# Kernel tuning notes

Measured on AMD Instinct MI355X. Metric: run time of the kernel, lower is better.

## Reference

```python
import jax, jax.numpy as jnp
import numpy as np

KERNEL_SIZE = 5
PAD = (KERNEL_SIZE - 1) // 2  # 2
PATCH = KERNEL_SIZE ** 2      # 25


def _conv2d(x, w, b):
    # x: [B,C,H,W], w: [O,I,3,3] -> SAME conv, stride 1
    y = jax.lax.conv_general_dilated(
        x, w, window_strides=(1, 1), padding='SAME',
        dimension_numbers=('NCHW', 'OIHW', 'NCHW'))
    return y + b[None, :, None, None]


def setup_inputs() -> dict:
    key = jax.random.key(0)
    ks = jax.random.split(key, 8)
    B, C, H, W = 4, 64, 192, 192
    rate = 2
    hidden = C * rate ** 2            # 256
    out_ch = 3 * KERNEL_SIZE ** 2     # 75
    s = 0.05
    return {
        'feature_x': jax.random.normal(ks[0], (B, C, H, W), jnp.float32),
        'x': jax.random.normal(ks[1], (B, 3, H, W), jnp.float32),
        'W1': jax.random.normal(ks[2], (hidden, C, 3, 3), jnp.float32) * s,
        'b1': jnp.zeros((hidden,), jnp.float32),
        'W2': jax.random.normal(ks[3], (hidden, hidden, 3, 3), jnp.float32) * s,
        'b2': jnp.zeros((hidden,), jnp.float32),
        'W3': jax.random.normal(ks[4], (out_ch, hidden, 3, 3), jnp.float32) * s,
        'b3': jnp.zeros((out_ch,), jnp.float32),
    }


def reference(feature_x, x, W1, b1, W2, b2, W3, b3):
    B, _, H, W = x.shape
    # kernel prediction branch: [B, 3*k^2, H, W]
    ks = _conv2d(_conv2d(_conv2d(feature_x, W1, b1), W2, b2), W3, b3)
    # gather k x k neighborhood of x with zero padding -> [B,3,H,W,PATCH]
    xpad = jnp.pad(x, ((0, 0), (0, 0), (PAD, PAD), (PAD, PAD)))
    x_off = jnp.stack(
        [xpad[:, :, di:di + H, dj:dj + W]
         for di in range(KERNEL_SIZE) for dj in range(KERNEL_SIZE)],
        axis=-1)
    # reshape predicted kernels: channel c = patch_idx*3 + color
    kern = ks.reshape(B, PATCH, 3, H, W).transpose(0, 2, 3, 4, 1)  # [B,3,H,W,PATCH]
    # fused multiply-reduce over patch dimension
    out = jnp.sum(x_off * kern, axis=-1)  # [B,3,H,W]
    return out
```

## Files before the change

### kernel.cpp

```cpp
#include <hip/hip_runtime.h>
#include <hip/hip_bf16.h>
#include <stdint.h>

#define HW 192
#define PLANE (HW * HW)
#define PH 194
#define PPG (PH * PH)

typedef __attribute__((ext_vector_type(8))) short frag8;
typedef __attribute__((ext_vector_type(16))) float f32x16;
typedef unsigned short ushort_t;

__device__ __forceinline__ ushort_t b16(float v) {
    __hip_bfloat16 b = __float2bfloat16(v);
    return __builtin_bit_cast(ushort_t, b);
}
__device__ __forceinline__ float b16f(ushort_t u) {
    return __bfloat162float(__builtin_bit_cast(__hip_bfloat16, u));
}

__device__ __forceinline__ void gld_lds16(const ushort_t* g, ushort_t* s) {
    __builtin_amdgcn_global_load_lds(
        (const __attribute__((address_space(1))) uint32_t*)(const void*)g,
        (__attribute__((address_space(3))) uint32_t*)(void*)s, 16, 0, 0);
}

template<int N> __device__ __forceinline__ void vmcnt_wait() {
    static_assert(N == 0 || N == 6, "unsupported vmcnt");
    if constexpr (N == 0) asm volatile("s_waitcnt vmcnt(0)" ::: "memory");
    else if constexpr (N == 6) asm volatile("s_waitcnt vmcnt(6)" ::: "memory");
}

__global__ __launch_bounds__(256) void wtrans_kernel(
    const float* __restrict__ w, ushort_t* __restrict__ wt,
    int C_IN, int C_OUT, int NCHUNK, int OTC, int total)
{
    for (int idx = blockIdx.x * 256 + threadIdx.x; idx < total; idx += gridDim.x * 256) {
        int ic = idx & 7;
        int g = idx >> 3;
        int o = g % OTC; g /= OTC;
        int t = g % 10;  g /= 10;
        int c8 = g % NCHUNK;
        int ob = g / NCHUNK;
        int og = ob * OTC + o;
        float v = 0.f;
        if (t < 9 && og < C_OUT)
            v = w[((size_t)og * C_IN + c8 * 8 + ic) * 9 + t];
        wt[idx] = b16(v);
    }
}

__global__ __launch_bounds__(256) void packfx_kernel(
    const float* __restrict__ src, ushort_t* __restrict__ d,
    int nb, size_t bstr)
{
    int n = nb * 64 * PLANE;
    for (int idx = blockIdx.x * 256 + threadIdx.x; idx < n; idx += gridDim.x * 256) {
        int c = idx / PLANE;
        int p = idx - c * PLANE;
        int b = c >> 6, cc = c & 63;
        int y = p / HW, x = p - y * HW;
        size_t di = (size_t)b * bstr + ((size_t)(cc >> 3) * PPG + (size_t)(y + 1) * PH + (x + 1)) * 8 + (cc & 7);
        d[di] = b16(src[idx]);
    }
}

__global__ __launch_bounds__(256) void zborder_kernel(
    ushort_t* __restrict__ ph, int nchunks)
{
    int total = nchunks * 772;
    for (int i = blockIdx.x * 256 + threadIdx.x; i < total; i += gridDim.x * 256) {
        int chunk = i / 772, b = i - chunk * 772;
        int y, x;
        if (b < 194)      { y = 0;   x = b; }
        else if (b < 388) { y = 193; x = b - 194; }
        else { int r = b - 388; y = 1 + (r >> 1); x = (r & 1) ? 193 : 0; }
        size_t g = ((size_t)chunk * PPG + (size_t)y * PH + x) * 8;
        *(uint4*)&ph[g] = make_uint4(0, 0, 0, 0);
    }
}

template<int NCHUNK, int OTC, int MF, bool LAST>
__global__ __launch_bounds__(256) void conv_mfma(
    const ushort_t* __restrict__ inp, const ushort_t* __restrict__ wt,
    const float* __restrict__ bias, int c_out,
    ushort_t* __restrict__ outp, const float* __restrict__ xin,
    float* __restrict__ outf, size_t in_bstr, size_t out_bstr)
{
    constexpr int NF = OTC / 32;
    constexpr int TSY = 4 * MF;
    constexpr int HGR2 = (TSY + 2) * 34;
    constexpr int HITER = (MF == 4) ? 3 : 2;
    constexpr int HPADG = HITER * 4 * 64;
    constexpr int WGR = 10 * OTC;
    constexpr int WITER = (OTC == 64) ? 3 : 4;
    constexpr int WPADG = WITER * 4 * 64;
    static_assert(HITER + WITER == 6, "uniform vmcnt immediate");
    constexpr int SMEM_USH = 2 * HPADG * 8 + 2 * WPADG * 8;
    static_assert(!LAST || SMEM_USH >= 96 * 256, "ks tile must fit staging LDS");
    __shared__ ushort_t smem[SMEM_USH];
    ushort_t* s_x = smem;
    ushort_t* s_w = smem + 2 * HPADG * 8;

    const int tid = threadIdx.x;
    const int wv = tid >> 6;
    const int lane = tid & 63;
    const int ln31 = lane & 31;
    const int lhalf = lane >> 5;
    const int tx0 = (blockIdx.x % 6) * 32;
    const int ty0 = (blockIdx.x / 6) * TSY;
    const int ob = blockIdx.y;
    const int bz = blockIdx.z;

    const ushort_t* bin = inp + (size_t)bz * in_bstr;

    int pixbase[MF];
    #pragma unroll
    for (int mf = 0; mf < MF; ++mf)
        pixbase[mf] = ((wv * MF + mf) * 34 + ln31) * 8;

    int hof[5], wslot[5];
    #pragma unroll
    for (int ks = 0; ks < 5; ++ks) {
        int t = ks * 2 + lhalf;
        wslot[ks] = t;
        int te = t > 8 ? 8 : t;
        int dy = te >= 6 ? 2 : (te >= 3 ? 1 : 0);
        int dx = te - dy * 3;
        hof[ks] = (dy * 34 + dx) * 8;
    }

    f32x16 acc[MF][NF];
    #pragma unroll
    for (int mf = 0; mf < MF; ++mf)
        #pragma unroll
        for (int nf = 0; nf < NF; ++nf) {
            int o = ob * OTC + nf * 32 + ln31;
            float bv = (o < c_out) ? bias[o] : 0.f;
            #pragma unroll
            for (int r = 0; r < 16; ++r) acc[mf][nf][r] = bv;
        }

    const ushort_t* wbase = wt + (size_t)ob * NCHUNK * WGR * 8;

    auto stage = [&](int buf, int c8) {
        const ushort_t* ih = bin + (size_t)c8 * PPG * 8;
        ushort_t* dx = s_x + buf * (HPADG * 8);
        #pragma unroll
        for (int i = 0; i < HITER; ++i) {
            int j = wv * HITER + i;
            int hg = j * 64 + lane;
            int hgc = hg < HGR2 ? hg : HGR2 - 1;
            int r = hgc / 34, c = hgc - r * 34;
            size_t sg = ((size_t)(ty0 + r) * PH + (tx0 + c)) * 8;
            gld_lds16(&ih[sg], &dx[j * 64 * 8]);
        }
        const ushort_t* wch = wbase + (size_t)c8 * WGR * 8;
        ushort_t* dw = s_w + buf * (WPADG * 8);
        #pragma unroll
        for (int i = 0; i < WITER; ++i) {
            int j = wv * WITER + i;
            int wg = j * 64 + lane;
            int wgc = wg < WGR ? wg : WGR - 1;
            gld_lds16(&wch[(size_t)wgc * 8], &dw[j * 64 * 8]);
        }
    };

    stage(0, 0);
    if (NCHUNK > 1) stage(1, 1);
    vmcnt_wait<0>();
    __builtin_amdgcn_s_barrier();
    __builtin_amdgcn_sched_barrier(0);

    for (int c8 = 0; c8 < NCHUNK; ++c8) {
        const int cur = c8 & 1;
        const ushort_t* xh = s_x + cur * (HPADG * 8);
        const ushort_t* wh = s_w + cur * (WPADG * 8);
        #pragma unroll
        for (int ks = 0; ks < 5; ++ks) {
            frag8 bh[NF];
            #pragma unroll
            for (int nf = 0; nf < NF; ++nf)
                bh[nf] = *(const frag8*)&wh[(wslot[ks] * OTC + nf * 32 + ln31) * 8];
            #pragma unroll
            for (int mf = 0; mf < MF; ++mf) {
                frag8 ah = *(const frag8*)&xh[pixbase[mf] + hof[ks]];
                #pragma unroll
                for (int nf = 0; nf < NF; ++nf)
                    acc[mf][nf] = __builtin_amdgcn_mfma_f32_32x32x16_bf16(ah, bh[nf], acc[mf][nf], 0, 0, 0);
            }
        }
        if (c8 + 1 == NCHUNK) break;
        __builtin_amdgcn_sched_barrier(0);
        __builtin_amdgcn_s_barrier();
        if (c8 + 2 < NCHUNK) {
            stage(cur, c8 + 2);
            vmcnt_wait<6>();
        } else {
            vmcnt_wait<0>();
        }
        __builtin_amdgcn_s_barrier();
        __builtin_amdgcn_sched_barrier(0);
    }

    if constexpr (!LAST) {
        #pragma unroll
        for (int mf = 0; mf < MF; ++mf) {
            int gy = ty0 + wv * MF + mf;
            #pragma unroll
            for (int nf = 0; nf < NF; ++nf) {
                int o = ob * OTC + nf * 32 + ln31;
                if (o < c_out) {
                    #pragma unroll
                    for (int i = 0; i < 4; ++i) {
                        int px = tx0 + i * 8 + lhalf * 4;
                        ushort_t* bout = outp + (size_t)bz * out_bstr;
                        size_t g0 = ((size_t)(o >> 3) * PPG + (size_t)(gy + 1) * PH + (px + 1)) * 8 + (o & 7);
                        #pragma unroll
                        for (int r = 0; r < 4; ++r)
                            bout[g0 + (size_t)r * 8] = b16(acc[mf][nf][4 * i + r]);
                    }
                }
            }
        }
    } else {
        __builtin_amdgcn_s_barrier();
        #pragma unroll
        for (int mf = 0; mf < MF; ++mf) {
            int lrow = wv * MF + mf;
            #pragma unroll
            for (int nf = 0; nf < NF; ++nf) {
                int o = nf * 32 + ln31;
                #pragma unroll
                for (int i = 0; i < 4; ++i) {
                    int pbase = lrow * 32 + i * 8 + lhalf * 4;
                    #pragma unroll
                    for (int r = 0; r < 4; ++r) {
                        int p = pbase + r;
                        smem[o * 256 + (p ^ ((o & 7) << 2))] = b16(acc[mf][nf][4 * i + r]);
                    }
                }
            }
        }
        __builtin_amdgcn_s_barrier();
        const int p = tid;
        const int gy = ty0 + (p >> 5);
        const int gx = tx0 + (p & 31);
        const float* xb = xin + (size_t)bz * 3 * PLANE;
        float* ob = outf + (size_t)bz * 3 * PLANE;
        float a[3] = {0.f, 0.f, 0.f};
        #pragma unroll
        for (int pt = 0; pt < 25; ++pt) {
            const int di = pt / 5, dj = pt % 5;
            int yy = gy + di - 2, xx = gx + dj - 2;
            bool inb = (yy >= 0 && yy < HW && xx >= 0 && xx < HW);
            #pragma unroll
            for (int c = 0; c < 3; ++c) {
                int k = pt * 3 + c;
                float kv = b16f(smem[k * 256 + (p ^ ((k & 7) << 2))]);
                float xv = inb ? xb[(size_t)c * PLANE + yy * HW + xx] : 0.f;
                a[c] = fmaf(kv, xv, a[c]);
            }
        }
        #pragma unroll
        for (int c = 0; c < 3; ++c)
            ob[(size_t)c * PLANE + gy * HW + gx] = a[c];
    }
}

extern "C" void kernel_launch(void* const* d_in, const int* in_sizes, int n_in,
                              void* d_out, int out_size, void* d_ws, size_t ws_size,
                              hipStream_t stream) {
    const float* feature_x = (const float*)d_in[0];
    const float* x  = (const float*)d_in[1];
    const float* W1 = (const float*)d_in[2];
    const float* b1 = (const float*)d_in[3];
    const float* W2 = (const float*)d_in[4];
    const float* b2 = (const float*)d_in[5];
    const float* W3 = (const float*)d_in[6];
    const float* b3 = (const float*)d_in[7];
    float* out = (float*)d_out;

    const size_t PLN32 = (size_t)32 * PPG * 8;
    const size_t PLN8  = (size_t)8 * PPG * 8;
    const size_t W1SZ = 163840, W2SZ = 655360, W3SZ = 307200;
    const size_t WTOT = W1SZ + W2SZ + W3SZ;
    const size_t FULL4 = (8 * PLN32 + WTOT) * 2;
    const int NB = (ws_size >= FULL4) ? 4 : 2;

    ushort_t* y1 = (ushort_t*)d_ws;
    ushort_t* y2 = y1 + (size_t)NB * PLN32;
    ushort_t* wb = y2 + (size_t)NB * PLN32;
    ushort_t* w1 = wb;
    ushort_t* w2 = w1 + W1SZ;
    ushort_t* w3 = w2 + W2SZ;
    ushort_t* fx  = y2;

    dim3 blk(256);
    wtrans_kernel<<<256, blk, 0, stream>>>(W1, w1, 64, 256, 8, 64, (int)W1SZ);
    wtrans_kernel<<<256, blk, 0, stream>>>(W2, w2, 256, 256, 32, 64, (int)W2SZ);
    wtrans_kernel<<<256, blk, 0, stream>>>(W3, w3, 256, 75, 32, 96, (int)W3SZ);

    dim3 g12(72, 4, NB), g3(144, 1, NB);
    for (int bp = 0; bp < 4 / NB; ++bp) {
        const float* fxsrc = feature_x + (size_t)bp * NB * 64 * PLANE;
        const float* x_b   = x   + (size_t)bp * NB * 3 * PLANE;
        float* out_b       = out + (size_t)bp * NB * 3 * PLANE;
        zborder_kernel<<<97, blk, 0, stream>>>(y1, NB * 32);
        zborder_kernel<<<97, blk, 0, stream>>>(y2, NB * 32);
        packfx_kernel<<<1024, blk, 0, stream>>>(fxsrc, fx, NB, PLN8);
        conv_mfma< 8, 64, 4, false><<<g12, blk, 0, stream>>>(
            fx, w1, b1, 256, y1, nullptr, nullptr, PLN8, PLN32);
        conv_mfma<32, 64, 4, false><<<g12, blk, 0, stream>>>(
            y1, w2, b2, 256, y2, nullptr, nullptr, PLN32, PLN32);
        conv_mfma<32, 96, 2, true ><<<g3, blk, 0, stream>>>(
            y2, w3, b3, 75, nullptr, x_b, out_b, PLN32, 0);
    }
}
```

Baseline: 396.5 us.

## Reorganize conv K-dimension as 16 channels per tap instead of packed taps

Each MFMA K=16 slice now covers 16 input channels (two 8-channel planes, one per lane half) for a single 3x3 tap, instead of two taps of 8 channels. This removes the wasted padded tenth tap slot and halves the number of chunk iterations. Weights are re-laid out with a padded output stride (OTC+4) to reduce LDS bank conflicts and are single-buffered. Halo tiles are double-buffered with two planes per chunk. The cost is a larger halo footprint per stage and a weight load that must complete inside the barrier window, because weights are no longer prefetched ahead.

```diff
diff --git a/kernel.cpp b/kernel.cpp
--- a/kernel.cpp
+++ b/kernel.cpp
@@ -26,9 +26,10 @@
 }
 
 template<int N> __device__ __forceinline__ void vmcnt_wait() {
-    static_assert(N == 0 || N == 6, "unsupported vmcnt");
+    static_assert(N == 0 || N == 3 || N == 5, "unsupported vmcnt");
     if constexpr (N == 0) asm volatile("s_waitcnt vmcnt(0)" ::: "memory");
-    else if constexpr (N == 6) asm volatile("s_waitcnt vmcnt(6)" ::: "memory");
+    else if constexpr (N == 3) asm volatile("s_waitcnt vmcnt(3)" ::: "memory");
+    else if constexpr (N == 5) asm volatile("s_waitcnt vmcnt(5)" ::: "memory");
 }
 
 __global__ __launch_bounds__(256) void wtrans_kernel(
@@ -38,14 +39,15 @@
     for (int idx = blockIdx.x * 256 + threadIdx.x; idx < total; idx += gridDim.x * 256) {
         int ic = idx & 7;
         int g = idx >> 3;
-        int o = g % OTC; g /= OTC;
-        int t = g % 10;  g /= 10;
-        int c8 = g % NCHUNK;
+        int o = g % (OTC + 4); g /= (OTC + 4);
+        int h = g & 1; g >>= 1;
+        int t = g % 9; g /= 9;
+        int cc = g % NCHUNK;
         int ob = g / NCHUNK;
         int og = ob * OTC + o;
         float v = 0.f;
-        if (t < 9 && og < C_OUT)
-            v = w[((size_t)og * C_IN + c8 * 8 + ic) * 9 + t];
+        if (o < OTC && og < C_OUT)
+            v = w[((size_t)og * C_IN + cc * 16 + h * 8 + ic) * 9 + t];
         wt[idx] = b16(v);
     }
 }
@@ -89,18 +91,18 @@
 {
     constexpr int NF = OTC / 32;
     constexpr int TSY = 4 * MF;
-    constexpr int HGR2 = (TSY + 2) * 34;
-    constexpr int HITER = (MF == 4) ? 3 : 2;
-    constexpr int HPADG = HITER * 4 * 64;
-    constexpr int WGR = 10 * OTC;
-    constexpr int WITER = (OTC == 64) ? 3 : 4;
-    constexpr int WPADG = WITER * 4 * 64;
-    static_assert(HITER + WITER == 6, "uniform vmcnt immediate");
-    constexpr int SMEM_USH = 2 * HPADG * 8 + 2 * WPADG * 8;
-    static_assert(!LAST || SMEM_USH >= 96 * 256, "ks tile must fit staging LDS");
+    constexpr int HGR_P = (TSY + 2) * 34;
+    constexpr int HGR_T = 2 * HGR_P;
+    constexpr int HSLOT = (MF == 4) ? 20 : 12;
+    constexpr int HPW = HSLOT / 4;
+    constexpr int WOS = OTC + 4;
+    constexpr int WGR = 9 * 2 * WOS;
+    constexpr int WSLOT = (WGR + 63) / 64;
+    constexpr int SMEM_USH = (2 * HSLOT + WSLOT) * 64 * 8;
+    static_assert(!LAST || SMEM_USH >= 96 * 256, "ks tile must fit LDS");
     __shared__ ushort_t smem[SMEM_USH];
     ushort_t* s_x = smem;
-    ushort_t* s_w = smem + 2 * HPADG * 8;
+    ushort_t* s_w = smem + 2 * HSLOT * 64 * 8;
 
     const int tid = threadIdx.x;
     const int wv = tid >> 6;
@@ -117,18 +119,7 @@
     int pixbase[MF];
     #pragma unroll
     for (int mf = 0; mf < MF; ++mf)
-        pixbase[mf] = ((wv * MF + mf) * 34 + ln31) * 8;
-
-    int hof[5], wslot[5];
-    #pragma unroll
-    for (int ks = 0; ks < 5; ++ks) {
-        int t = ks * 2 + lhalf;
-        wslot[ks] = t;
-        int te = t > 8 ? 8 : t;
-        int dy = te >= 6 ? 2 : (te >= 3 ? 1 : 0);
-        int dx = te - dy * 3;
-        hof[ks] = (dy * 34 + dx) * 8;
-    }
+        pixbase[mf] = (lhalf * HGR_P + (wv * MF + mf) * 34 + ln31) * 8;
 
     f32x16 acc[MF][NF];
     #pragma unroll
@@ -143,60 +134,64 @@
 
     const ushort_t* wbase = wt + (size_t)ob * NCHUNK * WGR * 8;
 
-    auto stage = [&](int buf, int c8) {
-        const ushort_t* ih = bin + (size_t)c8 * PPG * 8;
-        ushort_t* dx = s_x + buf * (HPADG * 8);
-        #pragma unroll
-        for (int i = 0; i < HITER; ++i) {
-            int j = wv * HITER + i;
+    auto stage_halo = [&](int buf, int cc) {
+        const ushort_t* ih = bin + (size_t)(2 * cc) * PPG * 8;
+        ushort_t* dx = s_x + buf * (HSLOT * 64 * 8);
+        #pragma unroll
+        for (int i = 0; i < HPW; ++i) {
+            int j = wv * HPW + i;
             int hg = j * 64 + lane;
-            int hgc = hg < HGR2 ? hg : HGR2 - 1;
-            int r = hgc / 34, c = hgc - r * 34;
-            size_t sg = ((size_t)(ty0 + r) * PH + (tx0 + c)) * 8;
+            int hgc = hg < HGR_T ? hg : HGR_T - 1;
+            int pl = hgc / HGR_P;
+            int rem = hgc - pl * HGR_P;
+            int r = rem / 34, c = rem - r * 34;
+            size_t sg = ((size_t)pl * PPG + (size_t)(ty0 + r) * PH + (tx0 + c)) * 8;
             gld_lds16(&ih[sg], &dx[j * 64 * 8]);
         }
-        const ushort_t* wch = wbase + (size_t)c8 * WGR * 8;
-        ushort_t* dw = s_w + buf * (WPADG * 8);
-        #pragma unroll
-        for (int i = 0; i < WITER; ++i) {
-            int j = wv * WITER + i;
+    };
+    auto stage_w = [&](int cc) {
+        const ushort_t* wch = wbase + (size_t)cc * WGR * 8;
+        for (int j = wv; j < WSLOT; j += 4) {
             int wg = j * 64 + lane;
             int wgc = wg < WGR ? wg : WGR - 1;
-            gld_lds16(&wch[(size_t)wgc * 8], &dw[j * 64 * 8]);
+            gld_lds16(&wch[(size_t)wgc * 8], &s_w[j * 64 * 8]);
         }
     };
 
-    stage(0, 0);
-    if (NCHUNK > 1) stage(1, 1);
+    stage_halo(0, 0);
+    stage_w(0);
+    if (NCHUNK > 1) stage_halo(1, 1);
     vmcnt_wait<0>();
     __builtin_amdgcn_s_barrier();
     __builtin_amdgcn_sched_barrier(0);
 
-    for (int c8 = 0; c8 < NCHUNK; ++c8) {
-        const int cur = c8 & 1;
-        const ushort_t* xh = s_x + cur * (HPADG * 8);
-        const ushort_t* wh = s_w + cur * (WPADG * 8);
-        #pragma unroll
-        for (int ks = 0; ks < 5; ++ks) {
+    for (int cc = 0; cc < NCHUNK; ++cc) {
+        const int cur = cc & 1;
+        const ushort_t* xh = s_x + cur * (HSLOT * 64 * 8);
+        #pragma unroll
+        for (int t = 0; t < 9; ++t) {
+            const int hof = ((t / 3) * 34 + (t % 3)) * 8;
             frag8 bh[NF];
             #pragma unroll
             for (int nf = 0; nf < NF; ++nf)
-                bh[nf] = *(const frag8*)&wh[(wslot[ks] * OTC + nf * 32 + ln31) * 8];
+                bh[nf] = *(const frag8*)&s_w[((t * 2 + lhalf) * WOS + nf * 32 + ln31) * 8];
             #pragma unroll
             for (int mf = 0; mf < MF; ++mf) {
-                frag8 ah = *(const frag8*)&xh[pixbase[mf] + hof[ks]];
+                frag8 ah = *(const frag8*)&xh[pixbase[mf] + hof];
                 #pragma unroll
                 for (int nf = 0; nf < NF; ++nf)
                     acc[mf][nf] = __builtin_amdgcn_mfma_f32_32x32x16_bf16(ah, bh[nf], acc[mf][nf], 0, 0, 0);
             }
         }
-        if (c8 + 1 == NCHUNK) break;
+        if (cc + 1 == NCHUNK) break;
         __builtin_amdgcn_sched_barrier(0);
         __builtin_amdgcn_s_barrier();
-        if (c8 + 2 < NCHUNK) {
-            stage(cur, c8 + 2);
-            vmcnt_wait<6>();
+        if (cc + 2 < NCHUNK) {
+            stage_w(cc + 1);
+            stage_halo(cur, cc + 2);
+            vmcnt_wait<HPW>();
         } else {
+            stage_w(cc + 1);
             vmcnt_wait<0>();
         }
         __builtin_amdgcn_s_barrier();
@@ -247,7 +242,7 @@
         const int gy = ty0 + (p >> 5);
         const int gx = tx0 + (p & 31);
         const float* xb = xin + (size_t)bz * 3 * PLANE;
-        float* ob = outf + (size_t)bz * 3 * PLANE;
+        float* ob2 = outf + (size_t)bz * 3 * PLANE;
         float a[3] = {0.f, 0.f, 0.f};
         #pragma unroll
         for (int pt = 0; pt < 25; ++pt) {
@@ -264,7 +259,7 @@
         }
         #pragma unroll
         for (int c = 0; c < 3; ++c)
-            ob[(size_t)c * PLANE + gy * HW + gx] = a[c];
+            ob2[(size_t)c * PLANE + gy * HW + gx] = a[c];
     }
 }
 
@@ -283,7 +278,9 @@
 
     const size_t PLN32 = (size_t)32 * PPG * 8;
     const size_t PLN8  = (size_t)8 * PPG * 8;
-    const size_t W1SZ = 163840, W2SZ = 655360, W3SZ = 307200;
+    const size_t W1SZ = (size_t)4 * 4  * 9 * 2 * 68  * 8;
+    const size_t W2SZ = (size_t)4 * 16 * 9 * 2 * 68  * 8;
+    const size_t W3SZ = (size_t)1 * 16 * 9 * 2 * 100 * 8;
     const size_t WTOT = W1SZ + W2SZ + W3SZ;
     const size_t FULL4 = (8 * PLN32 + WTOT) * 2;
     const int NB = (ws_size >= FULL4) ? 4 : 2;
@@ -297,9 +294,9 @@
     ushort_t* fx  = y2;
 
     dim3 blk(256);
-    wtrans_kernel<<<256, blk, 0, stream>>>(W1, w1, 64, 256, 8, 64, (int)W1SZ);
-    wtrans_kernel<<<256, blk, 0, stream>>>(W2, w2, 256, 256, 32, 64, (int)W2SZ);
-    wtrans_kernel<<<256, blk, 0, stream>>>(W3, w3, 256, 75, 32, 96, (int)W3SZ);
+    wtrans_kernel<<<256, blk, 0, stream>>>(W1, w1, 64, 256, 4, 64, (int)W1SZ);
+    wtrans_kernel<<<256, blk, 0, stream>>>(W2, w2, 256, 256, 16, 64, (int)W2SZ);
+    wtrans_kernel<<<256, blk, 0, stream>>>(W3, w3, 256, 75, 16, 96, (int)W3SZ);
 
     dim3 g12(72, 4, NB), g3(144, 1, NB);
     for (int bp = 0; bp < 4 / NB; ++bp) {
@@ -309,11 +306,11 @@
         zborder_kernel<<<97, blk, 0, stream>>>(y1, NB * 32);
         zborder_kernel<<<97, blk, 0, stream>>>(y2, NB * 32);
         packfx_kernel<<<1024, blk, 0, stream>>>(fxsrc, fx, NB, PLN8);
-        conv_mfma< 8, 64, 4, false><<<g12, blk, 0, stream>>>(
+        conv_mfma< 4, 64, 4, false><<<g12, blk, 0, stream>>>(
             fx, w1, b1, 256, y1, nullptr, nullptr, PLN8, PLN32);
-        conv_mfma<32, 64, 4, false><<<g12, blk, 0, stream>>>(
+        conv_mfma<16, 64, 4, false><<<g12, blk, 0, stream>>>(
             y1, w2, b2, 256, y2, nullptr, nullptr, PLN32, PLN32);
-        conv_mfma<32, 96, 2, true ><<<g3, blk, 0, stream>>>(
+        conv_mfma<16, 96, 2, true ><<<g3, blk, 0, stream>>>(
             y2, w3, b3, 75, nullptr, x_b, out_b, PLN32, 0);
     }
 }
```

Result: faster. 370.9 us (-6.5%).
